# Optimization experiments

Measured on AMD Instinct MI355X. Metric: run time of the kernel, lower is better.

## Reference

```python
import jax, jax.numpy as jnp
import numpy as np

N = 10000        # nodes
E = 160000       # edges
C = 128          # channel multiplicity (128x0e input)
RBF = 20         # edge_attr_dim
HID = 32         # edge MLP hidden
WN = 3 * C       # tp.weight_numel: 3 uvu paths (0e x Y_l -> l), 128 weights each


def setup_inputs() -> dict:
    key = jax.random.key(0)
    ks = jax.random.split(key, 12)
    f = lambda k, s, sc=1.0: jax.random.normal(k, s, jnp.float32) * sc
    return {
        "node_feat": f(ks[0], (N, C)),
        "edge_attr": f(ks[1], (E, RBF)),
        "edge_rsh": f(ks[2], (E, 9)),
        "edge_index": jax.random.randint(ks[3], (2, E), 0, N),
        # mlp_edge_scalar: Linear(2C->32), Linear(32->WN)
        "Ws1": f(ks[4], (2 * C, HID), 1.0 / np.sqrt(2 * C)), "bs1": jnp.zeros((HID,), jnp.float32),
        "Ws2": f(ks[5], (HID, WN), 1.0 / np.sqrt(HID)), "bs2": jnp.zeros((WN,), jnp.float32),
        # mlp_edge_rbf: Linear(20->32), Linear(32->WN)
        "Wr1": f(ks[6], (RBF, HID), 1.0 / np.sqrt(RBF)), "br1": jnp.zeros((HID,), jnp.float32),
        "Wr2": f(ks[7], (HID, WN), 1.0 / np.sqrt(HID)), "br2": jnp.zeros((WN,), jnp.float32),
        "lin2_w0": f(ks[8], (C, C)), "lin2_b0": jnp.zeros((C,), jnp.float32),
        "lin2_w1": f(ks[9], (C, C)),
        "lin2_w2": f(ks[10], (C, C)),
    }


def reference(node_feat, edge_attr, edge_rsh, edge_index,
              Ws1, bs1, Ws2, bs2, Wr1, br1, Wr2, br2,
              lin2_w0, lin2_b0, lin2_w1, lin2_w2):
    src, dst = edge_index[0], edge_index[1]
    xi = node_feat[src]            # [E, C] gathered scalars (center node)
    xj = node_feat[dst]            # [E, C] gathered scalars (neighbor)

    # First-layer branch: inner_dot of pure scalars -> elementwise product;
    # slice [:, C:] is empty, so s0 = concat(x_i scalars, x_j scalars).
    s0 = jnp.concatenate([xi, xj], axis=-1)  # [E, 2C]

    silu = jax.nn.silu
    w_s = silu(s0 @ Ws1 + bs1) @ Ws2 + bs2            # [E, 3C]
    w_r = silu(edge_attr @ Wr1 + br1) @ Wr2 + br2      # [E, 3C]
    tpw = w_s * w_r                                    # gated tensor-product weights

    w0, w1, w2 = tpw[:, :C], tpw[:, C:2 * C], tpw[:, 2 * C:]
    y0, y1, y2 = edge_rsh[:, :1], edge_rsh[:, 1:4], edge_rsh[:, 4:9]

    # uvu tensor product: per edge, per channel u: w_l[u] * x[u] * Y_l[m]
    m0 = (w0 * xj) * y0                                        # [E, C]
    m1 = (w1 * xj)[:, :, None] * y1[:, None, :]                # [E, C, 3]
    m2 = (w2 * xj)[:, :, None] * y2[:, None, :]                # [E, C, 5]
    msg = jnp.concatenate(
        [m0, m1.reshape(-1, 3 * C), m2.reshape(-1, 5 * C)], axis=-1)  # [E, 9C]

    # scatter-add to destination (edge_index[0])
    accu = jax.ops.segment_sum(msg, src, num_segments=node_feat.shape[0])  # [N, 9C]

    # lin_node2: equivariant linear (per-l channel mixing, bias on scalars only)
    a0 = accu[:, :C]
    a1 = accu[:, C:4 * C].reshape(-1, C, 3)
    a2 = accu[:, 4 * C:].reshape(-1, C, 5)
    inv = 1.0 / np.sqrt(C)  # e3nn o3.Linear fan-in normalization
    o0 = a0 @ lin2_w0 * inv + lin2_b0
    o1 = jnp.einsum('ncm,cd->ndm', a1, lin2_w1) * inv
    o2 = jnp.einsum('ncm,cd->ndm', a2, lin2_w2) * inv
    return jnp.concatenate([o0, o1.reshape(-1, 3 * C), o2.reshape(-1, 5 * C)], axis=-1)
```

## Files before the change

kernel.cpp:

```cpp
#include <hip/hip_runtime.h>
#include <hip/hip_bf16.h>
#include <math.h>

#define NN   10000
#define EE   160000
#define CC   128
#define RBFD 20
#define HIDD 32
#define WND  384
#define MROW 1152
#define EPB  64

typedef _Float16 half2_t __attribute__((ext_vector_type(2)));

__device__ __forceinline__ half2_t u2h(unsigned int u)
{
    union { unsigned int u; half2_t h; } c; c.u = u; return c.h;
}
__device__ __forceinline__ unsigned int pack_h2(float a, float b)
{
    union { half2_t h; unsigned int u; } c;
    c.h.x = (_Float16)a; c.h.y = (_Float16)b; return c.u;
}

__device__ __align__(16) float g_proj[(size_t)NN * 64];
__device__ __align__(16) float g_accu[(size_t)NN * MROW];
__device__ int g_deg[NN];
__device__ int g_offs[NN + 1];
__device__ int g_rel[EE];
__device__ int g_ord[EE];

__device__ __forceinline__ float silu_f(float x) { return x / (1.f + __expf(-x)); }

__global__ __launch_bounds__(256) void zero_kernel()
{
    int tid = blockIdx.x * 256 + threadIdx.x;
    if (tid < NN) g_deg[tid] = 0;
    float4* p = reinterpret_cast<float4*>(g_accu);
    float4 z = make_float4(0.f, 0.f, 0.f, 0.f);
    int n4 = NN * MROW / 4;
    for (int i = tid; i < n4; i += gridDim.x * 256) p[i] = z;
}

__global__ __launch_bounds__(256) void hist_kernel(const int* __restrict__ edge_index)
{
    int e = blockIdx.x * 256 + threadIdx.x;
    if (e < EE) g_rel[e] = atomicAdd(&g_deg[edge_index[e]], 1);
}

__global__ __launch_bounds__(256) void scan_kernel()
{
    __shared__ int sP[256];
    int t = threadIdx.x;
    int lo = t * 40, hi = min(lo + 40, NN);
    int sum = 0;
    for (int i = lo; i < hi; ++i) sum += g_deg[i];
    sP[t] = sum;
    __syncthreads();
    for (int off = 1; off < 256; off <<= 1) {
        int v = (t >= off) ? sP[t - off] : 0;
        __syncthreads();
        sP[t] += v;
        __syncthreads();
    }
    int run = sP[t] - sum;
    if (t == 0) g_offs[0] = 0;
    for (int i = lo; i < hi; ++i) { run += g_deg[i]; g_offs[i + 1] = run; }
}

__global__ __launch_bounds__(256) void perm_kernel(const int* __restrict__ edge_index)
{
    int e = blockIdx.x * 256 + threadIdx.x;
    if (e < EE) g_ord[g_offs[edge_index[e]] + g_rel[e]] = e;
}

__global__ __launch_bounds__(256) void proj_kernel(
    const float* __restrict__ nf,
    const float* __restrict__ Ws1, const float* __restrict__ bs1)
{
    __shared__ float sX[16][132];

    int tid = threadIdx.x;
    int nb = blockIdx.x * 16;

    #pragma unroll
    for (int i = tid; i < 512; i += 256) {
        int n = i >> 5, k4 = i & 31;
        float4 v = reinterpret_cast<const float4*>(nf + (size_t)(nb + n) * CC)[k4];
        sX[n][k4 * 4 + 0] = v.x;
        sX[n][k4 * 4 + 1] = v.y;
        sX[n][k4 * 4 + 2] = v.z;
        sX[n][k4 * 4 + 3] = v.w;
    }
    __syncthreads();

    int nl = tid >> 4;
    int qd = tid & 15;
    int j0 = (qd & 7) * 4;
    int rbase = (qd >= 8) ? CC : 0;

    float4 acc;
    if (qd < 8) acc = *reinterpret_cast<const float4*>(&bs1[j0]);
    else        acc = make_float4(0.f, 0.f, 0.f, 0.f);

    const float* wb = Ws1 + (size_t)rbase * HIDD + j0;
    #pragma unroll 4
    for (int k = 0; k < CC; ++k) {
        float f = sX[nl][k];
        float4 w = *reinterpret_cast<const float4*>(wb + (size_t)k * HIDD);
        acc.x = fmaf(f, w.x, acc.x);
        acc.y = fmaf(f, w.y, acc.y);
        acc.z = fmaf(f, w.z, acc.z);
        acc.w = fmaf(f, w.w, acc.w);
    }

    float* o = g_proj + (size_t)(nb + nl) * 64 + ((qd >= 8) ? HIDD : 0) + j0;
    *reinterpret_cast<float4*>(o) = acc;
}

template<int K, int YB, int MOFF>
__device__ __forceinline__ void section_pass(
    int sec, int l,
    const float2* __restrict__ nf2,
    const float* __restrict__ Ws2, const float* __restrict__ bs2,
    const float* __restrict__ Wr2, const float* __restrict__ br2,
    const unsigned int (*__restrict__ sH)[36], const float (*__restrict__ sY)[9],
    const int* __restrict__ sSrc, const int* __restrict__ sDst)
{
    unsigned int W0p[16], W1p[16], R0p[16], R1p[16];
    #pragma unroll
    for (int p = 0; p < 16; ++p) {
        int b0 = (2 * p) * WND + sec * 128 + 2 * l;
        int b1 = (2 * p + 1) * WND + sec * 128 + 2 * l;
        W0p[p] = pack_h2(Ws2[b0],     Ws2[b1]);
        W1p[p] = pack_h2(Ws2[b0 + 1], Ws2[b1 + 1]);
        R0p[p] = pack_h2(Wr2[b0],     Wr2[b1]);
        R1p[p] = pack_h2(Wr2[b0 + 1], Wr2[b1 + 1]);
    }
    #pragma unroll
    for (int p = 0; p < 16; ++p)
        asm volatile("" : "+v"(W0p[p]), "+v"(W1p[p]), "+v"(R0p[p]), "+v"(R1p[p]));

    float2 bsv = *reinterpret_cast<const float2*>(&bs2[sec * 128 + 2 * l]);
    float2 brv = *reinterpret_cast<const float2*>(&br2[sec * 128 + 2 * l]);

    float racc0[K], racc1[K];
    #pragma unroll
    for (int k = 0; k < K; ++k) { racc0[k] = 0.f; racc1[k] = 0.f; }
    int cur = sSrc[0];
    float2 xjn = nf2[(size_t)sDst[0] * 64 + l];

    #pragma unroll 2
    for (int ee = 0; ee < EPB; ++ee) {
        int src = sSrc[ee];
        if (src != cur) {
            float* ab = g_accu + (size_t)cur * MROW + MOFF + 2 * l;
            #pragma unroll
            for (int k = 0; k < K; ++k) {
                unsafeAtomicAdd(ab + k * CC,     racc0[k]);
                unsafeAtomicAdd(ab + k * CC + 1, racc1[k]);
                racc0[k] = 0.f; racc1[k] = 0.f;
            }
            cur = src;
        }
        float2 xj = xjn;
        xjn = nf2[(size_t)sDst[(ee + 1) & (EPB - 1)] * 64 + l];
        const uint4* hp = reinterpret_cast<const uint4*>(&sH[ee][0]);
        float as0 = bsv.x, as1 = bsv.y, ar0 = brv.x, ar1 = brv.y;
        #pragma unroll
        for (int q = 0; q < 4; ++q) {
            uint4 hv = hp[q];
            uint4 rv = hp[4 + q];
            as0 = __builtin_amdgcn_fdot2(u2h(hv.x), u2h(W0p[4 * q + 0]), as0, false);
            as1 = __builtin_amdgcn_fdot2(u2h(hv.x), u2h(W1p[4 * q + 0]), as1, false);
            as0 = __builtin_amdgcn_fdot2(u2h(hv.y), u2h(W0p[4 * q + 1]), as0, false);
            as1 = __builtin_amdgcn_fdot2(u2h(hv.y), u2h(W1p[4 * q + 1]), as1, false);
            as0 = __builtin_amdgcn_fdot2(u2h(hv.z), u2h(W0p[4 * q + 2]), as0, false);
            as1 = __builtin_amdgcn_fdot2(u2h(hv.z), u2h(W1p[4 * q + 2]), as1, false);
            as0 = __builtin_amdgcn_fdot2(u2h(hv.w), u2h(W0p[4 * q + 3]), as0, false);
            as1 = __builtin_amdgcn_fdot2(u2h(hv.w), u2h(W1p[4 * q + 3]), as1, false);
            ar0 = __builtin_amdgcn_fdot2(u2h(rv.x), u2h(R0p[4 * q + 0]), ar0, false);
            ar1 = __builtin_amdgcn_fdot2(u2h(rv.x), u2h(R1p[4 * q + 0]), ar1, false);
            ar0 = __builtin_amdgcn_fdot2(u2h(rv.y), u2h(R0p[4 * q + 1]), ar0, false);
            ar1 = __builtin_amdgcn_fdot2(u2h(rv.y), u2h(R1p[4 * q + 1]), ar1, false);
            ar0 = __builtin_amdgcn_fdot2(u2h(rv.z), u2h(R0p[4 * q + 2]), ar0, false);
            ar1 = __builtin_amdgcn_fdot2(u2h(rv.z), u2h(R1p[4 * q + 2]), ar1, false);
            ar0 = __builtin_amdgcn_fdot2(u2h(rv.w), u2h(R0p[4 * q + 3]), ar0, false);
            ar1 = __builtin_amdgcn_fdot2(u2h(rv.w), u2h(R1p[4 * q + 3]), ar1, false);
        }
        float u0 = as0 * ar0 * xj.x;
        float u1 = as1 * ar1 * xj.y;
        #pragma unroll
        for (int k = 0; k < K; ++k) {
            float yv = sY[ee][YB + k];
            racc0[k] = fmaf(u0, yv, racc0[k]);
            racc1[k] = fmaf(u1, yv, racc1[k]);
        }
    }
    float* ab = g_accu + (size_t)cur * MROW + MOFF + 2 * l;
    #pragma unroll
    for (int k = 0; k < K; ++k) {
        unsafeAtomicAdd(ab + k * CC,     racc0[k]);
        unsafeAtomicAdd(ab + k * CC + 1, racc1[k]);
    }
}

__global__ __launch_bounds__(64, 1) void fused_kernel(
    const float* __restrict__ nf,
    const float* __restrict__ edge_attr,
    const float* __restrict__ edge_rsh,
    const int*   __restrict__ edge_index,
    const float* __restrict__ Ws2, const float* __restrict__ bs2,
    const float* __restrict__ Wr1, const float* __restrict__ br1,
    const float* __restrict__ Wr2, const float* __restrict__ br2)
{
    __shared__ unsigned int sH[EPB][36];
    __shared__ float sY[EPB][9];
    __shared__ int   sSrc[EPB], sDst[EPB];

    int l = threadIdx.x;
    int p = blockIdx.x * EPB + l;
    int e = g_ord[p];
    int s = edge_index[e];
    int t = edge_index[EE + e];

    {
        float hs[HIDD], hr[HIDD];
        const float4* pi = reinterpret_cast<const float4*>(g_proj + (size_t)s * 64);
        const float4* pj = reinterpret_cast<const float4*>(g_proj + (size_t)t * 64 + HIDD);
        #pragma unroll
        for (int j4 = 0; j4 < HIDD / 4; ++j4) {
            float4 a = pi[j4], b = pj[j4];
            hs[4 * j4 + 0] = silu_f(a.x + b.x);
            hs[4 * j4 + 1] = silu_f(a.y + b.y);
            hs[4 * j4 + 2] = silu_f(a.z + b.z);
            hs[4 * j4 + 3] = silu_f(a.w + b.w);
        }
        #pragma unroll
        for (int j = 0; j < HIDD; ++j) hr[j] = br1[j];
        #pragma unroll 1
        for (int k4 = 0; k4 < RBFD / 4; ++k4) {
            float4 a = reinterpret_cast<const float4*>(edge_attr + (size_t)e * RBFD)[k4];
            const float* wp = Wr1 + (4 * k4) * HIDD;
            #pragma unroll
            for (int j = 0; j < HIDD; ++j) {
                hr[j] = fmaf(a.x, wp[j], hr[j]);
                hr[j] = fmaf(a.y, wp[HIDD + j], hr[j]);
                hr[j] = fmaf(a.z, wp[2 * HIDD + j], hr[j]);
                hr[j] = fmaf(a.w, wp[3 * HIDD + j], hr[j]);
            }
        }
        #pragma unroll
        for (int pp = 0; pp < 16; ++pp) {
            sH[l][pp]      = pack_h2(hs[2 * pp], hs[2 * pp + 1]);
            sH[l][16 + pp] = pack_h2(silu_f(hr[2 * pp]), silu_f(hr[2 * pp + 1]));
        }
        sSrc[l] = s;
        sDst[l] = t;
        #pragma unroll
        for (int i = 0; i < 9; ++i) sY[l][i] = edge_rsh[(size_t)e * 9 + i];
    }
    __syncthreads();

    const float2* nf2 = reinterpret_cast<const float2*>(nf);
    section_pass<1, 0, 0>     (0, l, nf2, Ws2, bs2, Wr2, br2, sH, sY, sSrc, sDst);
    section_pass<3, 1, CC>    (1, l, nf2, Ws2, bs2, Wr2, br2, sH, sY, sSrc, sDst);
    section_pass<5, 4, 4 * CC>(2, l, nf2, Ws2, bs2, Wr2, br2, sH, sY, sSrc, sDst);
}

__global__ __launch_bounds__(256) void lin2_kernel(
    const float* __restrict__ W0, const float* __restrict__ b0,
    const float* __restrict__ W1, const float* __restrict__ W2,
    float* __restrict__ out)
{
    __shared__ float sA[8 * MROW];
    int n0 = blockIdx.x * 8;
    const float4* g = reinterpret_cast<const float4*>(g_accu + (size_t)n0 * MROW);
    for (int i = threadIdx.x; i < 8 * MROW / 4; i += 256)
        reinterpret_cast<float4*>(sA)[i] = g[i];
    __syncthreads();

    int d  = threadIdx.x & (CC - 1);
    int nl = threadIdx.x >> 7;

    float acc[4][9];
    #pragma unroll
    for (int q = 0; q < 4; ++q)
        #pragma unroll
        for (int m = 0; m < 9; ++m) acc[q][m] = 0.f;

    #pragma unroll 1
    for (int c = 0; c < CC; ++c) {
        float w0 = W0[c * CC + d];
        float w1 = W1[c * CC + d];
        float w2 = W2[c * CC + d];
        #pragma unroll
        for (int q = 0; q < 4; ++q) {
            const float* a = sA + (size_t)(nl * 4 + q) * MROW;
            acc[q][0] = fmaf(a[c],          w0, acc[q][0]);
            acc[q][1] = fmaf(a[CC + c],     w1, acc[q][1]);
            acc[q][2] = fmaf(a[2 * CC + c], w1, acc[q][2]);
            acc[q][3] = fmaf(a[3 * CC + c], w1, acc[q][3]);
            acc[q][4] = fmaf(a[4 * CC + c], w2, acc[q][4]);
            acc[q][5] = fmaf(a[5 * CC + c], w2, acc[q][5]);
            acc[q][6] = fmaf(a[6 * CC + c], w2, acc[q][6]);
            acc[q][7] = fmaf(a[7 * CC + c], w2, acc[q][7]);
            acc[q][8] = fmaf(a[8 * CC + c], w2, acc[q][8]);
        }
    }

    const float inv = 0.08838834764831845f;
    #pragma unroll
    for (int q = 0; q < 4; ++q) {
        size_t ob = (size_t)(n0 + nl * 4 + q) * MROW;
        out[ob + d] = acc[q][0] * inv + b0[d];
        #pragma unroll
        for (int m = 0; m < 3; ++m) out[ob + CC + d * 3 + m]     = acc[q][1 + m] * inv;
        #pragma unroll
        for (int m = 0; m < 5; ++m) out[ob + 4 * CC + d * 5 + m] = acc[q][4 + m] * inv;
    }
}

extern "C" void kernel_launch(void* const* d_in, const int* in_sizes, int n_in,
                              void* d_out, int out_size, void* d_ws, size_t ws_size,
                              hipStream_t stream)
{
    const float* node_feat  = (const float*)d_in[0];
    const float* edge_attr  = (const float*)d_in[1];
    const float* edge_rsh   = (const float*)d_in[2];
    const int*   edge_index = (const int*)  d_in[3];
    const float* Ws1 = (const float*)d_in[4];
    const float* bs1 = (const float*)d_in[5];
    const float* Ws2 = (const float*)d_in[6];
    const float* bs2 = (const float*)d_in[7];
    const float* Wr1 = (const float*)d_in[8];
    const float* br1 = (const float*)d_in[9];
    const float* Wr2 = (const float*)d_in[10];
    const float* br2 = (const float*)d_in[11];
    const float* W0  = (const float*)d_in[12];
    const float* b0  = (const float*)d_in[13];
    const float* W1  = (const float*)d_in[14];
    const float* W2  = (const float*)d_in[15];
    float* out = (float*)d_out;

    zero_kernel<<<2048, 256, 0, stream>>>();
    hist_kernel<<<EE / 256, 256, 0, stream>>>(edge_index);
    scan_kernel<<<1, 256, 0, stream>>>();
    perm_kernel<<<EE / 256, 256, 0, stream>>>(edge_index);
    proj_kernel<<<NN / 16, 256, 0, stream>>>(node_feat, Ws1, bs1);
    fused_kernel<<<EE / EPB, 64, 0, stream>>>(
        node_feat, edge_attr, edge_rsh, edge_index,
        Ws2, bs2, Wr1, br1, Wr2, br2);
    lin2_kernel<<<NN / 8, 256, 0, stream>>>(W0, b0, W1, W2, out);
}
```

Before: 307.8 us.

## Split fused edge kernel across three wavefronts and fold permutation into proj kernel

The fused edge kernel now runs three wavefronts per block. The prologue is divided so one wave computes the scalar hidden features, one the RBF hidden features and one loads the spherical harmonics, and each wave then handles one of the three l-sections instead of one wave doing all three serially. The permutation scatter is merged into proj_kernel, which drops one launch. proj_kernel has NN/16=625 blocks of 256 threads, which exactly covers EE=160000 edges, so no bounds check is needed. The cost is more threads per block and possible imbalance between sections, since the l=2 section does five times the work of l=0.

```diff
diff --git a/kernel.cpp b/kernel.cpp
--- a/kernel.cpp
+++ b/kernel.cpp
@@ -68,20 +68,20 @@
     for (int i = lo; i < hi; ++i) { run += g_deg[i]; g_offs[i + 1] = run; }
 }
 
-__global__ __launch_bounds__(256) void perm_kernel(const int* __restrict__ edge_index)
-{
-    int e = blockIdx.x * 256 + threadIdx.x;
-    if (e < EE) g_ord[g_offs[edge_index[e]] + g_rel[e]] = e;
-}
-
 __global__ __launch_bounds__(256) void proj_kernel(
     const float* __restrict__ nf,
-    const float* __restrict__ Ws1, const float* __restrict__ bs1)
+    const float* __restrict__ Ws1, const float* __restrict__ bs1,
+    const int* __restrict__ edge_index)
 {
     __shared__ float sX[16][132];
 
     int tid = threadIdx.x;
     int nb = blockIdx.x * 16;
+
+    {
+        int eg = blockIdx.x * 256 + tid;
+        g_ord[g_offs[edge_index[eg]] + g_rel[eg]] = eg;
+    }
 
     #pragma unroll
     for (int i = tid; i < 512; i += 256) {
@@ -205,7 +205,7 @@
     }
 }
 
-__global__ __launch_bounds__(64, 1) void fused_kernel(
+__global__ __launch_bounds__(192, 1) void fused_kernel(
     const float* __restrict__ nf,
     const float* __restrict__ edge_attr,
     const float* __restrict__ edge_rsh,
@@ -218,24 +218,30 @@
     __shared__ float sY[EPB][9];
     __shared__ int   sSrc[EPB], sDst[EPB];
 
-    int l = threadIdx.x;
+    int tid = threadIdx.x;
+    int w = tid / 64;
+    int l = tid & 63;
     int p = blockIdx.x * EPB + l;
     int e = g_ord[p];
-    int s = edge_index[e];
-    int t = edge_index[EE + e];
-
-    {
-        float hs[HIDD], hr[HIDD];
+
+    if (w == 0) {
+        int s = edge_index[e];
+        int t = edge_index[EE + e];
         const float4* pi = reinterpret_cast<const float4*>(g_proj + (size_t)s * 64);
         const float4* pj = reinterpret_cast<const float4*>(g_proj + (size_t)t * 64 + HIDD);
         #pragma unroll
-        for (int j4 = 0; j4 < HIDD / 4; ++j4) {
-            float4 a = pi[j4], b = pj[j4];
-            hs[4 * j4 + 0] = silu_f(a.x + b.x);
-            hs[4 * j4 + 1] = silu_f(a.y + b.y);
-            hs[4 * j4 + 2] = silu_f(a.z + b.z);
-            hs[4 * j4 + 3] = silu_f(a.w + b.w);
-        }
+        for (int j4 = 0; j4 < HIDD / 8; ++j4) {
+            float4 a0 = pi[2 * j4],     b0 = pj[2 * j4];
+            float4 a1 = pi[2 * j4 + 1], b1 = pj[2 * j4 + 1];
+            sH[l][4 * j4 + 0] = pack_h2(silu_f(a0.x + b0.x), silu_f(a0.y + b0.y));
+            sH[l][4 * j4 + 1] = pack_h2(silu_f(a0.z + b0.z), silu_f(a0.w + b0.w));
+            sH[l][4 * j4 + 2] = pack_h2(silu_f(a1.x + b1.x), silu_f(a1.y + b1.y));
+            sH[l][4 * j4 + 3] = pack_h2(silu_f(a1.z + b1.z), silu_f(a1.w + b1.w));
+        }
+        sSrc[l] = s;
+        sDst[l] = t;
+    } else if (w == 1) {
+        float hr[HIDD];
         #pragma unroll
         for (int j = 0; j < HIDD; ++j) hr[j] = br1[j];
         #pragma unroll 1
@@ -251,21 +257,21 @@
             }
         }
         #pragma unroll
-        for (int pp = 0; pp < 16; ++pp) {
-            sH[l][pp]      = pack_h2(hs[2 * pp], hs[2 * pp + 1]);
+        for (int pp = 0; pp < 16; ++pp)
             sH[l][16 + pp] = pack_h2(silu_f(hr[2 * pp]), silu_f(hr[2 * pp + 1]));
-        }
-        sSrc[l] = s;
-        sDst[l] = t;
+    } else {
         #pragma unroll
         for (int i = 0; i < 9; ++i) sY[l][i] = edge_rsh[(size_t)e * 9 + i];
     }
     __syncthreads();
 
     const float2* nf2 = reinterpret_cast<const float2*>(nf);
-    section_pass<1, 0, 0>     (0, l, nf2, Ws2, bs2, Wr2, br2, sH, sY, sSrc, sDst);
-    section_pass<3, 1, CC>    (1, l, nf2, Ws2, bs2, Wr2, br2, sH, sY, sSrc, sDst);
-    section_pass<5, 4, 4 * CC>(2, l, nf2, Ws2, bs2, Wr2, br2, sH, sY, sSrc, sDst);
+    if (w == 0)
+        section_pass<1, 0, 0>     (0, l, nf2, Ws2, bs2, Wr2, br2, sH, sY, sSrc, sDst);
+    else if (w == 1)
+        section_pass<3, 1, CC>    (1, l, nf2, Ws2, bs2, Wr2, br2, sH, sY, sSrc, sDst);
+    else
+        section_pass<5, 4, 4 * CC>(2, l, nf2, Ws2, bs2, Wr2, br2, sH, sY, sSrc, sDst);
 }
 
 __global__ __launch_bounds__(256) void lin2_kernel(
@@ -346,9 +352,8 @@
     zero_kernel<<<2048, 256, 0, stream>>>();
     hist_kernel<<<EE / 256, 256, 0, stream>>>(edge_index);
     scan_kernel<<<1, 256, 0, stream>>>();
-    perm_kernel<<<EE / 256, 256, 0, stream>>>(edge_index);
-    proj_kernel<<<NN / 16, 256, 0, stream>>>(node_feat, Ws1, bs1);
-    fused_kernel<<<EE / EPB, 64, 0, stream>>>(
+    proj_kernel<<<NN / 16, 256, 0, stream>>>(node_feat, Ws1, bs1, edge_index);
+    fused_kernel<<<EE / EPB, 192, 0, stream>>>(
         node_feat, edge_attr, edge_rsh, edge_index,
         Ws2, bs2, Wr1, br1, Wr2, br2);
     lin2_kernel<<<NN / 8, 256, 0, stream>>>(W0, b0, W1, W2, out);
```

After: 284.3 us. 1.08x faster.
